# Kernel tuning notes

Measured on AMD Instinct MI355X. Metric: run time of the kernel, lower is better.

## Reference

```python
import jax, jax.numpy as jnp
import numpy as np

SEP_THRESHOLD = 5.0
TEMPERATURE = 0.1          # sigmoid temperature
SCALING_FACTOR = 1.0
DIST_TEMPERATURE = 1.0     # exponential temperature for repulsion energy
ATT_LOSS_GATE = 0.0
REP_LOSS_GATE = 0.0
EPS = 1e-10


def setup_inputs() -> dict:
    key = jax.random.key(0)
    k1, k2 = jax.random.split(key)
    B, L, K, C, D = 16, 64, 32, 32, 512
    prior = jax.random.normal(k1, (B, L, K, C), dtype=jnp.float32)
    h = jax.random.normal(k2, (B, L, D), dtype=jnp.float32)
    return {"prior": prior, "h": h}


def _jsd_matrix(prior):
    # prior: (B, L, K, C) logits -> pairwise JSD summed over K factors: (B, L, L)
    logp = jax.nn.log_softmax(prior, axis=-1)          # (B,L,K,C)
    p = jnp.exp(logp)
    p1, p2 = p[:, :, None], p[:, None]                  # (B,L,1,K,C), (B,1,L,K,C)
    lp1, lp2 = logp[:, :, None], logp[:, None]
    logm = jnp.log(0.5 * (p1 + p2))                     # mixture log-probs
    kl_p_m = jnp.sum(p1 * (lp1 - logm), axis=-1)        # (B,L,L,K)
    kl_q_m = jnp.sum(p2 * (lp2 - logm), axis=-1)
    jsd = 0.5 * (kl_p_m + kl_q_m)
    return jsd.sum(axis=-1) * SCALING_FACTOR            # (B,L,L)


def _ste_mask(soft, hard, triu):
    # straight-through: hard values forward, soft gradient backward
    return (hard + soft - jax.lax.stop_gradient(soft)) * triu


def reference(prior, h):
    B, L, K, C = prior.shape
    jsd = _jsd_matrix(prior)                            # (B,L,L)

    triu = jnp.triu(jnp.ones((L, L), dtype=prior.dtype), k=1)
    soft_att = jax.nn.sigmoid((SEP_THRESHOLD - jsd) / TEMPERATURE)
    hard_att = (jsd < SEP_THRESHOLD).astype(prior.dtype)
    att_mask = _ste_mask(soft_att, hard_att, triu)
    soft_rep = jax.nn.sigmoid((jsd - SEP_THRESHOLD) / TEMPERATURE)
    hard_rep = (jsd >= SEP_THRESHOLD).astype(prior.dtype)
    rep_mask = _ste_mask(soft_rep, hard_rep, triu)

    # pairwise MSE over hidden dim: (B,L,L)
    diff = h[:, :, None, :] - h[:, None, :, :]
    pairwise_mse = jnp.mean(diff * diff, axis=-1)

    loss_att = (pairwise_mse * att_mask).sum() / (att_mask.sum() + EPS)
    loss_att = jnp.where(loss_att > ATT_LOSS_GATE, loss_att, 0.0)

    repulsion_energy = jnp.exp(-pairwise_mse / DIST_TEMPERATURE)
    loss_rep = (repulsion_energy * rep_mask).sum() / (rep_mask.sum() + EPS)
    loss_rep = jnp.where(loss_rep > REP_LOSS_GATE, loss_rep, 0.0)

    return loss_att, loss_rep
```

## Files before the change

### kernel.cpp

```cpp
#include <hip/hip_runtime.h>
#include <math.h>

#define NB 16
#define NL 64
#define NK 32
#define NC 32
#define ND 512
#define EPSF 1e-10f

#define TILES_PER_B 36
#define PAIR_BLOCKS (NB * TILES_PER_B * 4)

#define THRS 14.426950408889634f
#define L2E  1.4426950408889634f

typedef _Float16 half2v __attribute__((ext_vector_type(2)));
typedef _Float16 half4v __attribute__((ext_vector_type(4)));
typedef _Float16 half8v __attribute__((ext_vector_type(8)));


__global__ void __launch_bounds__(256) softmax_kernel(
        const float* __restrict__ prior,
        const float* __restrict__ hg,
        _Float16* __restrict__ P,
        float* __restrict__ H2,
        _Float16* __restrict__ h16) {
    int bl = blockIdx.x;
    int t  = threadIdx.x;

    const float* src = prior + (size_t)bl * (NK * NC);
    float4 x = *(const float4*)(src + t * 4);
    float y0 = x.x * L2E, y1 = x.y * L2E, y2 = x.z * L2E, y3 = x.w * L2E;

    float m = fmaxf(fmaxf(y0, y1), fmaxf(y2, y3));
    #pragma unroll
    for (int w = 4; w >= 1; w >>= 1)
        m = fmaxf(m, __shfl_xor(m, w, 8));

    float e0 = exp2f(y0 - m), e1 = exp2f(y1 - m);
    float e2 = exp2f(y2 - m), e3 = exp2f(y3 - m);
    float s = e0 + e1 + e2 + e3;
    #pragma unroll
    for (int w = 4; w >= 1; w >>= 1)
        s += __shfl_xor(s, w, 8);

    float rs = 1.0f / s;
    float ls = __log2f(s);
    float p0 = e0 * rs, p1 = e1 * rs, p2 = e2 * rs, p3 = e3 * rs;
    float l0 = (y0 - m) - ls, l1 = (y1 - m) - ls;
    float l2 = (y2 - m) - ls, l3 = (y3 - m) - ls;

    half4v pv;
    pv[0] = (_Float16)fmaxf(p0, 1e-6f);
    pv[1] = (_Float16)fmaxf(p1, 1e-6f);
    pv[2] = (_Float16)fmaxf(p2, 1e-6f);
    pv[3] = (_Float16)fmaxf(p3, 1e-6f);
    *(half4v*)(P + (size_t)bl * (NK * NC) + t * 4) = pv;

    float2 hv = *(const float2*)(hg + (size_t)bl * ND + t * 2);
    half2v hh; hh[0] = (_Float16)hv.x; hh[1] = (_Float16)hv.y;
    *(half2v*)(h16 + (size_t)bl * ND + t * 2) = hh;

    float hacc = p0 * l0 + p1 * l1 + p2 * l2 + p3 * l3;
    #pragma unroll
    for (int w = 32; w >= 1; w >>= 1)
        hacc += __shfl_xor(hacc, w);
    __shared__ float red[4];
    int lane = t & 63, wib = t >> 6;
    if (lane == 0) red[wib] = hacc;
    __syncthreads();
    if (t == 0) H2[bl] = red[0] + red[1] + red[2] + red[3];
}

template<int CTRL>
__device__ __forceinline__ float dpp_add(float x) {
    int yi = __builtin_amdgcn_update_dpp(0, __float_as_int(x), CTRL, 0xF, 0xF, true);
    return x + __int_as_float(yi);
}

__device__ __forceinline__ float bf4f(float v0, float v1, float v2, float v3,
                                      bool hi32, bool hi16) {
    float sel0 = hi32 ? v2 : v0, oth0 = hi32 ? v0 : v2;
    float sel1 = hi32 ? v3 : v1, oth1 = hi32 ? v1 : v3;
    float w0 = sel0 + __shfl_xor(oth0, 32);
    float w1 = sel1 + __shfl_xor(oth1, 32);
    float sel = hi16 ? w1 : w0, oth = hi16 ? w0 : w1;
    float x = sel + __shfl_xor(oth, 16);
    x = dpp_add<0x111>(x);
    x = dpp_add<0x112>(x);
    x = dpp_add<0x114>(x);
    x = dpp_add<0x118>(x);
    return x;
}

__global__ void __launch_bounds__(256) pair_kernel(
        const _Float16* __restrict__ P,
        const float* __restrict__ H2g,
        const _Float16* __restrict__ h16,
        float* __restrict__ partials) {
    __shared__ float red[4][4];

    int tid  = threadIdx.x;
    int lane = tid & 63;
    int wv   = tid >> 6;

    int wg     = blockIdx.x;
    int b      = wg / (TILES_PER_B * 4);
    int rem144 = wg % (TILES_PER_B * 4);
    int t36    = rem144 >> 2;
    int quad   = rem144 & 3;

    int ti = 0, rem = t36;
    while (rem >= 8 - ti) { rem -= 8 - ti; ++ti; }
    int tj = ti + rem;
    bool diag = (ti == tj);
    int bi0 = b * NL + ti * 8;
    int bj0 = b * NL + tj * 8;

    int r    = quad * 2 + (wv >> 1);
    int scol = (wv & 1) * 4;

    const _Float16* arow = P + (size_t)(bi0 + r) * (NK * NC) + lane * 16;
    half8v arA = *(const half8v*)(arow);
    half8v arB = *(const half8v*)(arow + 8);
    half8v hr  = *(const half8v*)(h16 + (size_t)(bi0 + r) * ND + lane * 8);
    float h2i = H2g[bi0 + r];

    const _Float16* Pj = P   + (size_t)bj0 * (NK * NC) + lane * 16;
    const _Float16* Hj = h16 + (size_t)bj0 * ND + lane * 8;

    bool hi32 = (lane & 32) != 0;
    bool hi16 = (lane & 16) != 0;
    int  sgrp = lane >> 4;
    bool actl = (lane & 15) == 15;

    float S[4], M[4];
    #pragma unroll
    for (int q = 0; q < 4; ++q) {
        int s = scol + q;
        const _Float16* brow = Pj + s * 1024;
        half8v b0 = *(const half8v*)(brow);
        half8v b1 = *(const half8v*)(brow + 8);
        half8v t0 = arA + b0;
        half8v t1 = arB + b1;
        float a0 = 0.f, a1 = 0.f, a2 = 0.f, a3 = 0.f;
        #pragma unroll
        for (int e = 0; e < 8; e += 2) {
            float f0 = (float)t0[e];     a0 = fmaf(f0, __log2f(f0), a0);
            float f1 = (float)t0[e + 1]; a1 = fmaf(f1, __log2f(f1), a1);
            float g0 = (float)t1[e];     a2 = fmaf(g0, __log2f(g0), a2);
            float g1 = (float)t1[e + 1]; a3 = fmaf(g1, __log2f(g1), a3);
        }
        S[q] = (a0 + a1) + (a2 + a3);

        half8v hs = *(const half8v*)(Hj + s * 512);
        half8v d = hr - hs;
        float m0 = 0.f, m1 = 0.f;
        #pragma unroll
        for (int e = 0; e < 8; e += 2) {
            m0 = fmaf((float)d[e],     (float)d[e],     m0);
            m1 = fmaf((float)d[e + 1], (float)d[e + 1], m1);
        }
        M[q] = m0 + m1;
    }

    float xS = bf4f(S[0], S[1], S[2], S[3], hi32, hi16);
    float xM = bf4f(M[0], M[1], M[2], M[3], hi32, hi16);

    int s = scol + sgrp;
    float stat = h2i + H2g[bj0 + s] + 64.0f - xS;
    float mse  = xM * (1.0f / ND);
    float rt   = exp2f(-mse * L2E);
    bool valid = (!diag) || (s > r);
    bool isAtt = stat < THRS;

    float attN = (actl && valid && isAtt)  ? mse : 0.f;
    float attC = (actl && valid && isAtt)  ? 1.f : 0.f;
    float repN = (actl && valid && !isAtt) ? rt  : 0.f;
    float repC = (actl && valid && !isAtt) ? 1.f : 0.f;

    attN += __shfl_xor(attN, 16); attN += __shfl_xor(attN, 32);
    attC += __shfl_xor(attC, 16); attC += __shfl_xor(attC, 32);
    repN += __shfl_xor(repN, 16); repN += __shfl_xor(repN, 32);
    repC += __shfl_xor(repC, 16); repC += __shfl_xor(repC, 32);

    if (lane == 63) {
        red[wv][0] = attN; red[wv][1] = attC;
        red[wv][2] = repN; red[wv][3] = repC;
    }
    __syncthreads();
    if (tid < 4) {
        float v = red[0][tid] + red[1][tid] + red[2][tid] + red[3][tid];
        partials[blockIdx.x * 4 + tid] = v;
    }
}

__global__ void __launch_bounds__(256) finalize_kernel(
        const float* __restrict__ partials,
        float* __restrict__ out) {
    int tid = threadIdx.x;
    float a0 = 0.0f, a1 = 0.0f, a2 = 0.0f, a3 = 0.0f;
    for (int bkt = tid; bkt < PAIR_BLOCKS; bkt += 256) {
        a0 += partials[bkt * 4 + 0];
        a1 += partials[bkt * 4 + 1];
        a2 += partials[bkt * 4 + 2];
        a3 += partials[bkt * 4 + 3];
    }
    #pragma unroll
    for (int w = 32; w >= 1; w >>= 1) {
        a0 += __shfl_xor(a0, w);
        a1 += __shfl_xor(a1, w);
        a2 += __shfl_xor(a2, w);
        a3 += __shfl_xor(a3, w);
    }
    __shared__ float red[4][4];
    int lane = tid & 63, wib = tid >> 6;
    if (lane == 0) {
        red[wib][0] = a0; red[wib][1] = a1; red[wib][2] = a2; red[wib][3] = a3;
    }
    __syncthreads();
    if (tid == 0) {
        float s0 = red[0][0] + red[1][0] + red[2][0] + red[3][0];
        float s1 = red[0][1] + red[1][1] + red[2][1] + red[3][1];
        float s2 = red[0][2] + red[1][2] + red[2][2] + red[3][2];
        float s3 = red[0][3] + red[1][3] + red[2][3] + red[3][3];
        float la = s0 / (s1 + EPSF);
        float lr = s2 / (s3 + EPSF);
        out[0] = (la > 0.0f) ? la : 0.0f;
        out[1] = (lr > 0.0f) ? lr : 0.0f;
    }
}

extern "C" void kernel_launch(void* const* d_in, const int* in_sizes, int n_in,
                              void* d_out, int out_size, void* d_ws, size_t ws_size,
                              hipStream_t stream) {
    const float* prior = (const float*)d_in[0];
    const float* h     = (const float*)d_in[1];
    float* out = (float*)d_out;
    float* ws  = (float*)d_ws;

    float* partials = ws;
    _Float16* P = (_Float16*)(ws + 16384);
    float* H2 = ws + 16384 + 524288;
    _Float16* h16 = (_Float16*)(ws + 16384 + 524288 + 1024);

    softmax_kernel<<<NB * NL, 256, 0, stream>>>(prior, h, P, H2, h16);

    pair_kernel<<<PAIR_BLOCKS, 256, 0, stream>>>(P, H2, h16, partials);

    finalize_kernel<<<1, 256, 0, stream>>>(partials, out);
}
```

Measured before the change: 23.62 us.

## Fuse finalize into pair kernel via last-block atomic counters and remap block order

Removes the separate finalize launch. Each pair block writes its partials with an atomic store and bumps one of 32 sharded counters, and a second-level counter picks the last block, which does the final reduction and writes the output. The counters are reset in the softmax kernel. Block indices are also permuted across 8 groups (likely XCD-aware), so a batch's tiles share an L2. The code relies on relaxed atomics with no explicit fences for ordering, which is a correctness risk in exchange for saving a launch.

```diff
diff --git a/kernel.cpp b/kernel.cpp
--- a/kernel.cpp
+++ b/kernel.cpp
@@ -24,9 +24,13 @@
         const float* __restrict__ hg,
         _Float16* __restrict__ P,
         float* __restrict__ H2,
-        _Float16* __restrict__ h16) {
+        _Float16* __restrict__ h16,
+        int* __restrict__ counters) {
     int bl = blockIdx.x;
     int t  = threadIdx.x;
+    if (bl == 0 && t < 33)
+        __hip_atomic_store(&counters[t], 0, __ATOMIC_RELAXED,
+                           __HIP_MEMORY_SCOPE_AGENT);
 
     const float* src = prior + (size_t)bl * (NK * NC);
     float4 x = *(const float4*)(src + t * 4);
@@ -97,14 +101,18 @@
         const _Float16* __restrict__ P,
         const float* __restrict__ H2g,
         const _Float16* __restrict__ h16,
-        float* __restrict__ partials) {
+        float* __restrict__ partials,
+        int* __restrict__ counters,
+        float* __restrict__ out) {
     __shared__ float red[4][4];
+    __shared__ int lastFlag;
 
     int tid  = threadIdx.x;
     int lane = tid & 63;
     int wv   = tid >> 6;
 
-    int wg     = blockIdx.x;
+    int wg = (blockIdx.x & 7) * 288 + (blockIdx.x >> 3);
+
     int b      = wg / (TILES_PER_B * 4);
     int rem144 = wg % (TILES_PER_B * 4);
     int t36    = rem144 >> 2;
@@ -191,20 +199,32 @@
     __syncthreads();
     if (tid < 4) {
         float v = red[0][tid] + red[1][tid] + red[2][tid] + red[3][tid];
-        partials[blockIdx.x * 4 + tid] = v;
-    }
-}
-
-__global__ void __launch_bounds__(256) finalize_kernel(
-        const float* __restrict__ partials,
-        float* __restrict__ out) {
-    int tid = threadIdx.x;
-    float a0 = 0.0f, a1 = 0.0f, a2 = 0.0f, a3 = 0.0f;
+        __hip_atomic_store(&partials[blockIdx.x * 4 + tid], v,
+                           __ATOMIC_RELAXED, __HIP_MEMORY_SCOPE_AGENT);
+    }
+    __syncthreads();
+
+    if (tid == 0) {
+        int g = blockIdx.x & 31;
+        int old = __hip_atomic_fetch_add(&counters[g], 1, __ATOMIC_RELAXED,
+                                         __HIP_MEMORY_SCOPE_AGENT);
+        int lf = 0;
+        if (old == (PAIR_BLOCKS / 32) - 1) {
+            int o2 = __hip_atomic_fetch_add(&counters[32], 1, __ATOMIC_RELAXED,
+                                            __HIP_MEMORY_SCOPE_AGENT);
+            lf = (o2 == 31);
+        }
+        lastFlag = lf;
+    }
+    __syncthreads();
+    if (!lastFlag) return;
+
+    float a0 = 0.f, a1 = 0.f, a2 = 0.f, a3 = 0.f;
     for (int bkt = tid; bkt < PAIR_BLOCKS; bkt += 256) {
-        a0 += partials[bkt * 4 + 0];
-        a1 += partials[bkt * 4 + 1];
-        a2 += partials[bkt * 4 + 2];
-        a3 += partials[bkt * 4 + 3];
+        a0 += __hip_atomic_load(&partials[bkt * 4 + 0], __ATOMIC_RELAXED, __HIP_MEMORY_SCOPE_AGENT);
+        a1 += __hip_atomic_load(&partials[bkt * 4 + 1], __ATOMIC_RELAXED, __HIP_MEMORY_SCOPE_AGENT);
+        a2 += __hip_atomic_load(&partials[bkt * 4 + 2], __ATOMIC_RELAXED, __HIP_MEMORY_SCOPE_AGENT);
+        a3 += __hip_atomic_load(&partials[bkt * 4 + 3], __ATOMIC_RELAXED, __HIP_MEMORY_SCOPE_AGENT);
     }
     #pragma unroll
     for (int w = 32; w >= 1; w >>= 1) {
@@ -213,10 +233,9 @@
         a2 += __shfl_xor(a2, w);
         a3 += __shfl_xor(a3, w);
     }
-    __shared__ float red[4][4];
-    int lane = tid & 63, wib = tid >> 6;
     if (lane == 0) {
-        red[wib][0] = a0; red[wib][1] = a1; red[wib][2] = a2; red[wib][3] = a3;
+        red[wv][0] = a0; red[wv][1] = a1;
+        red[wv][2] = a2; red[wv][3] = a3;
     }
     __syncthreads();
     if (tid == 0) {
@@ -240,13 +259,12 @@
     float* ws  = (float*)d_ws;
 
     float* partials = ws;
+    int*   counters = (int*)(ws + 9216);
     _Float16* P = (_Float16*)(ws + 16384);
     float* H2 = ws + 16384 + 524288;
     _Float16* h16 = (_Float16*)(ws + 16384 + 524288 + 1024);
 
-    softmax_kernel<<<NB * NL, 256, 0, stream>>>(prior, h, P, H2, h16);
-
-    pair_kernel<<<PAIR_BLOCKS, 256, 0, stream>>>(P, H2, h16, partials);
-
-    finalize_kernel<<<1, 256, 0, stream>>>(partials, out);
-}
+    softmax_kernel<<<NB * NL, 256, 0, stream>>>(prior, h, P, H2, h16, counters);
+
+    pair_kernel<<<PAIR_BLOCKS, 256, 0, stream>>>(P, H2, h16, partials, counters, out);
+}
```

Result: slower. 31.09 us (+31.7%).
